# Kernel optimization log

Hardware: AMD Instinct MI355X
Metric: run time of the kernel (lower is better)

The kernel has to match this reference:

```python
import jax, jax.numpy as jnp
import numpy as np

USER_NUM = 100000
ITEM_NUM = 100000
DIM = 64
BS = 256


def setup_inputs() -> dict:
    key = jax.random.key(0)
    k1, k2, k3, k4, k5 = jax.random.split(key, 5)
    # xavier_normal-ish scale for embeddings/linear
    user_table = jax.random.normal(k1, (USER_NUM, DIM), dtype=jnp.float32) * 0.1
    item_table = jax.random.normal(k2, (ITEM_NUM, DIM), dtype=jnp.float32) * 0.1
    cls_w = jax.random.normal(k3, (5, DIM), dtype=jnp.float32) * (2.0 / (DIM + 5)) ** 0.5
    cls_b = jnp.zeros((5,), dtype=jnp.float32)
    batch_user = jax.random.randint(k4, (BS,), 0, USER_NUM, dtype=jnp.int64)
    values = jnp.array([[1.0, 2.0, 3.0, 4.0, 5.0]], dtype=jnp.float32)
    return {
        "batch_user": batch_user,
        "user_table": user_table,
        "item_table": item_table,
        "cls_w": cls_w,
        "cls_b": cls_b,
        "values": values,
    }


def reference(batch_user, user_table, item_table, cls_w, cls_b, values):
    # forward_full_items: score every (user, item) pair.
    # Torch materializes h_ui = (u repeated) * (items tiled) of shape
    # [bs*item_num, dim]; mathematically logits = einsum over dim, so we
    # fuse the broadcasted product with the tiny Linear to avoid the
    # huge expanded intermediate while computing identical math.
    u = user_table[batch_user]                       # [bs, dim]
    # logits[b,i,c] = sum_d u[b,d] * item[i,d] * W[c,d] + b[c]
    logits = jnp.einsum('bd,id,cd->bic', u, item_table, cls_w) + cls_b  # [bs, item_num, 5]
    prob = jax.nn.softmax(logits, axis=-1)
    return jnp.sum(prob * values[0], axis=-1)        # [bs, item_num]
```

## Files before the change

kernel.cpp:

```cpp
#include <hip/hip_runtime.h>

#define I_TOTAL 100000
#define DIM 64
#define BS 256

typedef __attribute__((ext_vector_type(8))) short bf16x8;
typedef __attribute__((ext_vector_type(4))) float f32x4;

__device__ inline unsigned short f2bf(float x) {
    union { float f; unsigned u; } v; v.f = x;
    return (unsigned short)((v.u + 0x8000u) >> 16);
}

__global__ __launch_bounds__(256) void prep_M(
    const int* __restrict__ bu, const float* __restrict__ ut,
    const float* __restrict__ cw, unsigned short* __restrict__ Mbf)
{
    int idx = blockIdx.x * 256 + threadIdx.x;
    int d = (idx & 15) * 4;
    int n = idx >> 4;
    int c = n >> 8, b = n & 255;
    const float s = 1.4426950408889634f;
    float4 u = *(const float4*)(ut + (long)bu[b] * DIM + d);
    float4 w = *(const float4*)(cw + c * DIM + d);
    ushort4 r;
    r.x = f2bf(u.x * w.x * s);
    r.y = f2bf(u.y * w.y * s);
    r.z = f2bf(u.z * w.z * s);
    r.w = f2bf(u.w * w.w * s);
    *(ushort4*)(Mbf + n * DIM + d) = r;
}

__global__ __launch_bounds__(256) void conv_items(
    const float* __restrict__ item, unsigned short* __restrict__ itbf)
{
    long t = (long)blockIdx.x * 256 + threadIdx.x;
    const float4* p = (const float4*)(item + t * 8);
    float4 a = p[0], b = p[1];
    ushort4 r0, r1;
    r0.x = f2bf(a.x); r0.y = f2bf(a.y); r0.z = f2bf(a.z); r0.w = f2bf(a.w);
    r1.x = f2bf(b.x); r1.y = f2bf(b.y); r1.z = f2bf(b.z); r1.w = f2bf(b.w);
    ushort4* q = (ushort4*)(itbf + t * 8);
    q[0] = r0; q[1] = r1;
}

template <bool PRE>
__global__ __launch_bounds__(256) void gemm_softmax(
    const float* __restrict__ item, const unsigned short* __restrict__ itbf,
    const unsigned short* __restrict__ Mbf,
    const float* __restrict__ clsb, const float* __restrict__ vals,
    float* __restrict__ out)
{
    const int lane = threadIdx.x & 63;
    const int wave = threadIdx.x >> 6;
    const int col  = lane & 15;
    const int quad = lane >> 4;

    const int  b_base = blockIdx.x * 16;
    const long i_wave = (long)blockIdx.y * 256 + wave * 64;

    bf16x8 afr[5][2];
#pragma unroll
    for (int c = 0; c < 5; ++c) {
        const unsigned short* p = Mbf + (c * BS + b_base + col) * DIM + quad * 8;
        afr[c][0] = *(const bf16x8*)p;
        afr[c][1] = *(const bf16x8*)(p + 32);
    }

    f32x4 acc[5][4];
#pragma unroll
    for (int c = 0; c < 5; ++c)
#pragma unroll
        for (int t = 0; t < 4; ++t)
            acc[c][t] = (f32x4){0.f, 0.f, 0.f, 0.f};

#pragma unroll
    for (int t = 0; t < 4; ++t) {
        long i  = i_wave + t * 16 + col;
        long ic = (i < I_TOTAL) ? i : (I_TOTAL - 1);
        bf16x8 b0, b1;
        if constexpr (PRE) {
            const unsigned short* rp = itbf + ic * DIM + quad * 8;
            b0 = *(const bf16x8*)rp;
            b1 = *(const bf16x8*)(rp + 32);
        } else {
            const float4* fp = (const float4*)(item + ic * DIM);
            float4 q0 = fp[2 * quad];
            float4 q1 = fp[2 * quad + 1];
            float4 q2 = fp[8 + 2 * quad];
            float4 q3 = fp[8 + 2 * quad + 1];
            b0[0] = (short)f2bf(q0.x); b0[1] = (short)f2bf(q0.y);
            b0[2] = (short)f2bf(q0.z); b0[3] = (short)f2bf(q0.w);
            b0[4] = (short)f2bf(q1.x); b0[5] = (short)f2bf(q1.y);
            b0[6] = (short)f2bf(q1.z); b0[7] = (short)f2bf(q1.w);
            b1[0] = (short)f2bf(q2.x); b1[1] = (short)f2bf(q2.y);
            b1[2] = (short)f2bf(q2.z); b1[3] = (short)f2bf(q2.w);
            b1[4] = (short)f2bf(q3.x); b1[5] = (short)f2bf(q3.y);
            b1[6] = (short)f2bf(q3.z); b1[7] = (short)f2bf(q3.w);
        }
#pragma unroll
        for (int c = 0; c < 5; ++c) {
            acc[c][t] = __builtin_amdgcn_mfma_f32_16x16x32_bf16(afr[c][0], b0, acc[c][t], 0, 0, 0);
            acc[c][t] = __builtin_amdgcn_mfma_f32_16x16x32_bf16(afr[c][1], b1, acc[c][t], 0, 0, 0);
        }
    }

    const float s = 1.4426950408889634f;
    float bb[5], vv[5];
#pragma unroll
    for (int c = 0; c < 5; ++c) { bb[c] = clsb[c] * s; vv[c] = vals[c]; }

#pragma unroll
    for (int t = 0; t < 4; ++t) {
        long i = i_wave + t * 16 + col;
        if (i >= I_TOTAL) continue;
#pragma unroll
        for (int r = 0; r < 4; ++r) {
            int b = b_base + quad * 4 + r;
            float num = 0.f, den = 0.f;
#pragma unroll
            for (int c = 0; c < 5; ++c) {
                float e = exp2f(acc[c][t][r] + bb[c]);
                den += e;
                num += e * vv[c];
            }
            out[(long)b * I_TOTAL + i] = num * __builtin_amdgcn_rcpf(den);
        }
    }
}

extern "C" void kernel_launch(void* const* d_in, const int* in_sizes, int n_in,
                              void* d_out, int out_size, void* d_ws, size_t ws_size,
                              hipStream_t stream) {
    const int*   bu   = (const int*)d_in[0];
    const float* ut   = (const float*)d_in[1];
    const float* it   = (const float*)d_in[2];
    const float* cw   = (const float*)d_in[3];
    const float* cb   = (const float*)d_in[4];
    const float* vals = (const float*)d_in[5];
    float* out = (float*)d_out;
    unsigned short* Mbf = (unsigned short*)d_ws;
    unsigned short* itbf = (unsigned short*)((char*)d_ws + 163840);

    const size_t needed = 163840 + (size_t)I_TOTAL * DIM * 2;

    prep_M<<<80, 256, 0, stream>>>(bu, ut, cw, Mbf);
    dim3 grid(16, 391);
    if (ws_size >= needed) {
        conv_items<<<3125, 256, 0, stream>>>(it, itbf);
        gemm_softmax<true><<<grid, 256, 0, stream>>>(it, itbf, Mbf, cb, vals, out);
    } else {
        gemm_softmax<false><<<grid, 256, 0, stream>>>(it, itbf, Mbf, cb, vals, out);
    }
}
```

Baseline: 192.2 us.

## Enlarge per-block item tile, swizzle block order, and stream MFMA+softmax per subtile

The main GEMM+softmax kernel now gives each block 1024 items (256 per wave) instead of 256 items, and runs a 1D grid with a swizzled mapping that groups 8 item-tiles across the 16 batch groups. The A fragments are loaded once and reused over many more item subtiles. Accumulators are now computed and consumed per 16-item subtile instead of holding 20 accumulators, which lowers register pressure. A bounds-free fast path covers full tiles, and a clamped path handles the tail. The intent is to cut per-block setup overhead, improve L2 locality for item reads, and raise occupancy, at the cost of fewer blocks and less parallelism per launch.

```diff
diff --git a/kernel.cpp b/kernel.cpp
--- a/kernel.cpp
+++ b/kernel.cpp
@@ -44,20 +44,27 @@
     q[0] = r0; q[1] = r1;
 }
 
-template <bool PRE>
 __global__ __launch_bounds__(256) void gemm_softmax(
-    const float* __restrict__ item, const unsigned short* __restrict__ itbf,
+    const unsigned short* __restrict__ itbf,
     const unsigned short* __restrict__ Mbf,
     const float* __restrict__ clsb, const float* __restrict__ vals,
     float* __restrict__ out)
 {
+    const int blk = blockIdx.x;
+    const int r8 = blk & 7;
+    const int q  = blk >> 3;
+    const int g  = q & 15;
+    const int a  = q >> 4;
+    const int y  = a * 8 + r8;
+    if (y >= 98) return;
+
     const int lane = threadIdx.x & 63;
     const int wave = threadIdx.x >> 6;
     const int col  = lane & 15;
     const int quad = lane >> 4;
 
-    const int  b_base = blockIdx.x * 16;
-    const long i_wave = (long)blockIdx.y * 256 + wave * 64;
+    const int b_base = g * 16;
+    const int i_base = y * 1024 + wave * 256;
 
     bf16x8 afr[5][2];
 #pragma unroll
@@ -67,49 +74,134 @@
         afr[c][1] = *(const bf16x8*)(p + 32);
     }
 
+    const f32x4 zero = (f32x4){0.f, 0.f, 0.f, 0.f};
+
+    const float s = 1.4426950408889634f;
+    float bb[5], vv[5];
+#pragma unroll
+    for (int c = 0; c < 5; ++c) { bb[c] = clsb[c] * s; vv[c] = vals[c]; }
+
+    if (y < 97) {
+        float* op[4];
+#pragma unroll
+        for (int rr = 0; rr < 4; ++rr)
+            op[rr] = out + (size_t)(b_base + quad * 4 + rr) * I_TOTAL + (i_base + col);
+
+        const unsigned short* bp = itbf + (size_t)(i_base + col) * DIM + quad * 8;
+
+#pragma unroll 1
+        for (int t4 = 0; t4 < 4; ++t4) {
+#pragma unroll
+            for (int ti = 0; ti < 4; ++ti) {
+                bf16x8 b0 = *(const bf16x8*)(bp + ti * 1024);
+                bf16x8 b1 = *(const bf16x8*)(bp + ti * 1024 + 32);
+                f32x4 acc[5];
+#pragma unroll
+                for (int c = 0; c < 5; ++c) {
+                    acc[c] = __builtin_amdgcn_mfma_f32_16x16x32_bf16(afr[c][0], b0, zero, 0, 0, 0);
+                    acc[c] = __builtin_amdgcn_mfma_f32_16x16x32_bf16(afr[c][1], b1, acc[c], 0, 0, 0);
+                }
+#pragma unroll
+                for (int rr = 0; rr < 4; ++rr) {
+                    float e0 = exp2f(acc[0][rr] + bb[0]);
+                    float e1 = exp2f(acc[1][rr] + bb[1]);
+                    float e2 = exp2f(acc[2][rr] + bb[2]);
+                    float e3 = exp2f(acc[3][rr] + bb[3]);
+                    float e4 = exp2f(acc[4][rr] + bb[4]);
+                    float den = ((e0 + e1) + (e2 + e3)) + e4;
+                    float num = e0 * vv[0];
+                    num = fmaf(e1, vv[1], num);
+                    num = fmaf(e2, vv[2], num);
+                    num = fmaf(e3, vv[3], num);
+                    num = fmaf(e4, vv[4], num);
+                    op[rr][ti * 16] = num * __builtin_amdgcn_rcpf(den);
+                }
+            }
+            bp += 4 * 1024;
+#pragma unroll
+            for (int rr = 0; rr < 4; ++rr) op[rr] += 64;
+        }
+    } else {
+#pragma unroll 1
+        for (int t = 0; t < 16; ++t) {
+            int i  = i_base + t * 16 + col;
+            int ic = i < I_TOTAL ? i : I_TOTAL - 1;
+            const unsigned short* p2 = itbf + (size_t)ic * DIM + quad * 8;
+            bf16x8 b0 = *(const bf16x8*)p2;
+            bf16x8 b1 = *(const bf16x8*)(p2 + 32);
+            f32x4 acc[5];
+#pragma unroll
+            for (int c = 0; c < 5; ++c) {
+                acc[c] = __builtin_amdgcn_mfma_f32_16x16x32_bf16(afr[c][0], b0, zero, 0, 0, 0);
+                acc[c] = __builtin_amdgcn_mfma_f32_16x16x32_bf16(afr[c][1], b1, acc[c], 0, 0, 0);
+            }
+            if (i < I_TOTAL) {
+#pragma unroll
+                for (int rr = 0; rr < 4; ++rr) {
+                    float e0 = exp2f(acc[0][rr] + bb[0]);
+                    float e1 = exp2f(acc[1][rr] + bb[1]);
+                    float e2 = exp2f(acc[2][rr] + bb[2]);
+                    float e3 = exp2f(acc[3][rr] + bb[3]);
+                    float e4 = exp2f(acc[4][rr] + bb[4]);
+                    float den = ((e0 + e1) + (e2 + e3)) + e4;
+                    float num = e0 * vv[0];
+                    num = fmaf(e1, vv[1], num);
+                    num = fmaf(e2, vv[2], num);
+                    num = fmaf(e3, vv[3], num);
+                    num = fmaf(e4, vv[4], num);
+                    out[(size_t)(b_base + quad * 4 + rr) * I_TOTAL + i] =
+                        num * __builtin_amdgcn_rcpf(den);
+                }
+            }
+        }
+    }
+}
+
+__global__ __launch_bounds__(256) void gemm_softmax_fb(
+    const float* __restrict__ item, const unsigned short* __restrict__ Mbf,
+    const float* __restrict__ clsb, const float* __restrict__ vals,
+    float* __restrict__ out)
+{
+    const int lane = threadIdx.x & 63;
+    const int wave = threadIdx.x >> 6;
+    const int col  = lane & 15;
+    const int quad = lane >> 4;
+    const int  b_base = blockIdx.x * 16;
+    const long i_wave = (long)blockIdx.y * 256 + wave * 64;
+
+    bf16x8 afr[5][2];
+#pragma unroll
+    for (int c = 0; c < 5; ++c) {
+        const unsigned short* p = Mbf + (c * BS + b_base + col) * DIM + quad * 8;
+        afr[c][0] = *(const bf16x8*)p;
+        afr[c][1] = *(const bf16x8*)(p + 32);
+    }
     f32x4 acc[5][4];
 #pragma unroll
     for (int c = 0; c < 5; ++c)
 #pragma unroll
-        for (int t = 0; t < 4; ++t)
-            acc[c][t] = (f32x4){0.f, 0.f, 0.f, 0.f};
-
+        for (int t = 0; t < 4; ++t) acc[c][t] = (f32x4){0.f,0.f,0.f,0.f};
 #pragma unroll
     for (int t = 0; t < 4; ++t) {
         long i  = i_wave + t * 16 + col;
         long ic = (i < I_TOTAL) ? i : (I_TOTAL - 1);
+        const float4* fp = (const float4*)(item + ic * DIM);
+        float4 q0 = fp[2*quad], q1 = fp[2*quad+1], q2 = fp[8+2*quad], q3 = fp[8+2*quad+1];
         bf16x8 b0, b1;
-        if constexpr (PRE) {
-            const unsigned short* rp = itbf + ic * DIM + quad * 8;
-            b0 = *(const bf16x8*)rp;
-            b1 = *(const bf16x8*)(rp + 32);
-        } else {
-            const float4* fp = (const float4*)(item + ic * DIM);
-            float4 q0 = fp[2 * quad];
-            float4 q1 = fp[2 * quad + 1];
-            float4 q2 = fp[8 + 2 * quad];
-            float4 q3 = fp[8 + 2 * quad + 1];
-            b0[0] = (short)f2bf(q0.x); b0[1] = (short)f2bf(q0.y);
-            b0[2] = (short)f2bf(q0.z); b0[3] = (short)f2bf(q0.w);
-            b0[4] = (short)f2bf(q1.x); b0[5] = (short)f2bf(q1.y);
-            b0[6] = (short)f2bf(q1.z); b0[7] = (short)f2bf(q1.w);
-            b1[0] = (short)f2bf(q2.x); b1[1] = (short)f2bf(q2.y);
-            b1[2] = (short)f2bf(q2.z); b1[3] = (short)f2bf(q2.w);
-            b1[4] = (short)f2bf(q3.x); b1[5] = (short)f2bf(q3.y);
-            b1[6] = (short)f2bf(q3.z); b1[7] = (short)f2bf(q3.w);
-        }
+        b0[0]=(short)f2bf(q0.x); b0[1]=(short)f2bf(q0.y); b0[2]=(short)f2bf(q0.z); b0[3]=(short)f2bf(q0.w);
+        b0[4]=(short)f2bf(q1.x); b0[5]=(short)f2bf(q1.y); b0[6]=(short)f2bf(q1.z); b0[7]=(short)f2bf(q1.w);
+        b1[0]=(short)f2bf(q2.x); b1[1]=(short)f2bf(q2.y); b1[2]=(short)f2bf(q2.z); b1[3]=(short)f2bf(q2.w);
+        b1[4]=(short)f2bf(q3.x); b1[5]=(short)f2bf(q3.y); b1[6]=(short)f2bf(q3.z); b1[7]=(short)f2bf(q3.w);
 #pragma unroll
         for (int c = 0; c < 5; ++c) {
             acc[c][t] = __builtin_amdgcn_mfma_f32_16x16x32_bf16(afr[c][0], b0, acc[c][t], 0, 0, 0);
             acc[c][t] = __builtin_amdgcn_mfma_f32_16x16x32_bf16(afr[c][1], b1, acc[c][t], 0, 0, 0);
         }
     }
-
     const float s = 1.4426950408889634f;
     float bb[5], vv[5];
 #pragma unroll
     for (int c = 0; c < 5; ++c) { bb[c] = clsb[c] * s; vv[c] = vals[c]; }
-
 #pragma unroll
     for (int t = 0; t < 4; ++t) {
         long i = i_wave + t * 16 + col;
@@ -121,8 +213,7 @@
 #pragma unroll
             for (int c = 0; c < 5; ++c) {
                 float e = exp2f(acc[c][t][r] + bb[c]);
-                den += e;
-                num += e * vv[c];
+                den += e; num = fmaf(e, vv[c], num);
             }
             out[(long)b * I_TOTAL + i] = num * __builtin_amdgcn_rcpf(den);
         }
@@ -139,17 +230,17 @@
     const float* cb   = (const float*)d_in[4];
     const float* vals = (const float*)d_in[5];
     float* out = (float*)d_out;
-    unsigned short* Mbf = (unsigned short*)d_ws;
+    unsigned short* Mbf  = (unsigned short*)d_ws;
     unsigned short* itbf = (unsigned short*)((char*)d_ws + 163840);
 
     const size_t needed = 163840 + (size_t)I_TOTAL * DIM * 2;
 
     prep_M<<<80, 256, 0, stream>>>(bu, ut, cw, Mbf);
-    dim3 grid(16, 391);
     if (ws_size >= needed) {
         conv_items<<<3125, 256, 0, stream>>>(it, itbf);
-        gemm_softmax<true><<<grid, 256, 0, stream>>>(it, itbf, Mbf, cb, vals, out);
+        gemm_softmax<<<1664, 256, 0, stream>>>(itbf, Mbf, cb, vals, out);
     } else {
-        gemm_softmax<false><<<grid, 256, 0, stream>>>(it, itbf, Mbf, cb, vals, out);
-    }
-}
+        dim3 grid(16, 391);
+        gemm_softmax_fb<<<grid, 256, 0, stream>>>(it, Mbf, cb, vals, out);
+    }
+}
```

Result: faster. 187.1 us (-2.7%).
